# Optimization experiments

Hardware: AMD Instinct MI355X
Metric: run time of the kernel (lower is better)

The kernel has to match this reference:

```python
import jax, jax.numpy as jnp
import numpy as np

T, IN, INTER, OUT = 4096, 1024, 1024, 1024

def setup_inputs() -> dict:
    key = jax.random.key(0)
    ks = jax.random.split(key, 11)
    s_in = 1.0 / np.sqrt(IN)
    s_int = 1.0 / np.sqrt(INTER)
    return {
        "x": jax.random.normal(ks[0], (T, IN), dtype=jnp.float32),
        "d_gamma": jax.random.uniform(ks[1], (T, T), dtype=jnp.float32),
        "Wq": jax.random.uniform(ks[2], (IN, INTER), jnp.float32, -s_in, s_in),
        "bq": jax.random.uniform(ks[3], (INTER,), jnp.float32, -s_in, s_in),
        "Wk": jax.random.uniform(ks[4], (IN, INTER), jnp.float32, -s_in, s_in),
        "bk": jax.random.uniform(ks[5], (INTER,), jnp.float32, -s_in, s_in),
        "Wv": jax.random.uniform(ks[6], (IN, INTER), jnp.float32, -s_in, s_in),
        "bv": jax.random.uniform(ks[7], (INTER,), jnp.float32, -s_in, s_in),
        "Wr": jax.random.uniform(ks[8], (INTER, OUT), jnp.float32, -s_int, s_int),
        "br": jax.random.uniform(ks[9], (OUT,), jnp.float32, -s_int, s_int),
        "prelu_a": jnp.asarray(0.25, dtype=jnp.float32),
    }

def reference(x, d_gamma, Wq, bq, Wk, bk, Wv, bv, Wr, br, prelu_a):
    num_node = x.shape[0]
    xr = x.reshape(T, IN)
    q = xr @ Wq + bq                      # [T, INTER]
    k = xr @ Wk + bk                      # [T, INTER]
    v = xr @ Wv + bv                      # [T, INTER]
    scores = q @ k.T                      # [T, T] retention scores
    retained = (d_gamma * scores) @ v     # decay-masked aggregation, [T, INTER]
    out = retained @ Wr + br              # [T, OUT]
    out = jnp.where(out >= 0, out, prelu_a * out)  # PReLU
    return out.reshape(num_node, -1)
```

## Files before the change

kernel.cpp:

```cpp
#include <hip/hip_runtime.h>

#define TT 4096
#define DIN 1024

typedef _Float16 f16;
typedef __attribute__((ext_vector_type(8))) _Float16 f16x8;
typedef __attribute__((ext_vector_type(4))) _Float16 f16x4;
typedef __attribute__((ext_vector_type(4))) float f32x4;

__device__ f16 g_xh[TT * DIN];
__device__ f16 g_wqkvT[3 * DIN * DIN];
__device__ f16 g_wrT[DIN * DIN];
__device__ f16 g_q[TT * DIN];
__device__ f16 g_k[TT * DIN];
__device__ f16 g_v[TT * DIN];
__device__ f16 g_vT[DIN * TT];
__device__ f16 g_sg[(size_t)TT * TT];
__device__ f16 g_part[4][TT * DIN];
__device__ f16 g_ret[TT * DIN];

__global__ __launch_bounds__(256) void prep_cast_x(const float* __restrict__ x) {
    int i = (blockIdx.x * 256 + threadIdx.x) * 8;
    f32x4 a = *(const f32x4*)&x[i];
    f32x4 b = *(const f32x4*)&x[i + 4];
    f16x8 o;
#pragma unroll
    for (int j = 0; j < 4; ++j) { o[j] = (f16)a[j]; o[j + 4] = (f16)b[j]; }
    *(f16x8*)&g_xh[i] = o;
}

__global__ __launch_bounds__(256) void prep_transpose(const float* __restrict__ Wq,
                                                      const float* __restrict__ Wk,
                                                      const float* __restrict__ Wv,
                                                      const float* __restrict__ Wr) {
    __shared__ float tt[64][68];
    const int which = blockIdx.z;
    const float* src = (which == 0) ? Wq : (which == 1) ? Wk : (which == 2) ? Wv : Wr;
    f16* dst = (which < 3) ? (g_wqkvT + (size_t)which * DIN * DIN) : g_wrT;
    const int t = threadIdx.x;
    const int r = t >> 2;
    const int c0 = (t & 3) * 4;
#pragma unroll
    for (int ch = 0; ch < 4; ++ch)
        *(f32x4*)&tt[r][c0 + ch * 16] =
            *(const f32x4*)&src[(size_t)(blockIdx.y * 64 + r) * DIN + blockIdx.x * 64 + c0 + ch * 16];
    __syncthreads();
#pragma unroll
    for (int p = 0; p < 2; ++p) {
        const int j  = (t >> 3) + p * 32;
        const int k0 = (t & 7) * 8;
        f16x8 o;
#pragma unroll
        for (int jj = 0; jj < 8; ++jj) o[jj] = (f16)tt[k0 + jj][j];
        *(f16x8*)&dst[(size_t)(blockIdx.x * 64 + j) * DIN + blockIdx.y * 64 + k0] = o;
    }
}

__global__ __launch_bounds__(256) void transpose_v() {
    __shared__ f16 t[64][72];
    const int bc = blockIdx.x;
    const int br = blockIdx.y;
    const int tdx = threadIdx.x;
    const int r0 = tdx >> 3;
    const int c8 = (tdx & 7) * 8;
#pragma unroll
    for (int p = 0; p < 2; ++p) {
        int r = r0 + p * 32;
        *(f16x8*)&t[r][c8] = *(const f16x8*)&g_v[(size_t)(br * 64 + r) * DIN + bc * 64 + c8];
    }
    __syncthreads();
#pragma unroll
    for (int p = 0; p < 2; ++p) {
        int c = r0 + p * 32;
        f16x8 v;
#pragma unroll
        for (int j = 0; j < 8; ++j) v[j] = t[c8 + j][c];
        *(f16x8*)&g_vT[(size_t)(bc * 64 + c) * TT + br * 64 + c8] = v;
    }
}

__device__ __forceinline__ void gload_lds16(const void* g, void* l) {
    __builtin_amdgcn_global_load_lds(
        (const __attribute__((address_space(1))) unsigned int*)g,
        (__attribute__((address_space(3))) unsigned int*)l,
        16, 0, 0);
}

template <int EPI>
__global__ __launch_bounds__(512, 2) void gemm8(const float* __restrict__ gamma,
                                                const float* __restrict__ bq,
                                                const float* __restrict__ bk,
                                                const float* __restrict__ bv) {
    constexpr int NT  = (EPI == 3) ? 4 : 16;
    constexpr int ld2A = (EPI == 2) ? 8192 : 2048;
    constexpr int ld2B = (EPI == 2) ? 8192 : 2048;

    const f16* Ap = (EPI == 0) ? g_xh : (EPI == 1) ? g_q : (EPI == 2) ? g_sg : g_ret;
    const f16* Bp = (EPI == 0) ? g_wqkvT : (EPI == 1) ? g_k : (EPI == 2) ? g_vT : g_wrT;
    const int kb_base = (EPI == 2) ? blockIdx.z * 2048
                      : (EPI == 3) ? blockIdx.z * 512 : 0;

    __shared__ __align__(16) char smem[131072];

    const int t = threadIdx.x;
    const int w = t >> 6, l = t & 63;
    const int wr = w >> 2, wc = w & 3;
    const int fr = l & 15;
    const int fkb = (l >> 4) * 16;

    const int nx = gridDim.x;
    const int lin = blockIdx.y * nx + blockIdx.x;
    const int cpx = (nx * gridDim.y) >> 3;
    const int sw = (lin & 7) * cpx + (lin >> 3);
    const int bx = sw % nx, by = sw / nx;
    const int arow0 = by * 256;
    const int bcol0 = bx * 256;

    auto stage = [&](const f16* M, int ld2, int row0, int kb0, int dstoff) {
#pragma unroll
        for (int r = 0; r < 2; ++r) {
            int off = r * 8192 + w * 1024;
            int row = (off + l * 16) >> 7;
            int cb  = (l & 7) * 16;
            int scb = cb ^ ((row & 7) << 4);
            const char* src = (const char*)M + (size_t)(row0 + row) * ld2 + kb0 + scb;
            gload_lds16(src, smem + dstoff + off);
        }
    };

    auto ldsA = [&](int c, int m, int ks) -> f16x8 {
        int lr = m * 16 + fr;
        int kb = ks * 64 + fkb;
        return *(const f16x8*)(smem + c * 65536 + wr * 16384 + lr * 128 + (kb ^ ((lr & 7) << 4)));
    };
    auto ldsB = [&](int c, int n, int ks) -> f16x8 {
        int lc = (wc & 1) * 64 + n * 16 + fr;
        int kb = ks * 64 + fkb;
        return *(const f16x8*)(smem + c * 65536 + 32768 + (wc >> 1) * 16384 + lc * 128 + (kb ^ ((lc & 7) << 4)));
    };

#define KB(kt) (kb_base + (kt) * 128)

    stage(Ap, ld2A, arow0,       KB(0), 0);
    stage(Ap, ld2A, arow0 + 128, KB(0), 16384);
    stage(Bp, ld2B, bcol0,       KB(0), 32768);
    stage(Bp, ld2B, bcol0 + 128, KB(0), 49152);
    stage(Bp, ld2B, bcol0,       KB(1), 65536 + 32768);
    stage(Bp, ld2B, bcol0 + 128, KB(1), 65536 + 49152);

    f32x4 acc[8][4] = {};
    f16x8 bf[4][2];

#define GPHASE(MB, STAGE_STMT)                                              \
    {                                                                       \
        f16x8 af[2][2];                                                     \
        _Pragma("unroll") for (int i = 0; i < 2; ++i)                       \
            _Pragma("unroll") for (int ks = 0; ks < 2; ++ks)                \
                af[i][ks] = ldsA(c, (MB) + i, ks);                          \
        STAGE_STMT;                                                         \
        __builtin_amdgcn_s_barrier();                                       \
        __builtin_amdgcn_s_setprio(1);                                      \
        _Pragma("unroll") for (int i = 0; i < 2; ++i)                       \
            _Pragma("unroll") for (int n = 0; n < 4; ++n)                   \
                _Pragma("unroll") for (int ks = 0; ks < 2; ++ks)            \
                    acc[(MB) + i][n] = __builtin_amdgcn_mfma_f32_16x16x32_f16( \
                        af[i][ks], bf[n][ks], acc[(MB) + i][n], 0, 0, 0);   \
        __builtin_amdgcn_s_setprio(0);                                      \
        __builtin_amdgcn_s_barrier();                                       \
    }

    for (int kt = 0; kt < NT; ++kt) {
        const int c = kt & 1;
        if (kt == NT - 1) asm volatile("s_waitcnt vmcnt(0)" ::: "memory");
        else              asm volatile("s_waitcnt vmcnt(4)" ::: "memory");
        __builtin_amdgcn_s_barrier();
#pragma unroll
        for (int n = 0; n < 4; ++n)
#pragma unroll
            for (int ks = 0; ks < 2; ++ks) bf[n][ks] = ldsB(c, n, ks);
        GPHASE(0, if (kt + 1 < NT) stage(Ap, ld2A, arow0,       KB(kt + 1), (c ^ 1) * 65536))
        GPHASE(2, if (kt + 1 < NT) stage(Ap, ld2A, arow0 + 128, KB(kt + 1), (c ^ 1) * 65536 + 16384))
        GPHASE(4, if (kt + 2 < NT) stage(Bp, ld2B, bcol0,       KB(kt + 2), c * 65536 + 32768))
        GPHASE(6, if (kt + 2 < NT) stage(Bp, ld2B, bcol0 + 128, KB(kt + 2), c * 65536 + 49152))
    }
#undef GPHASE
#undef KB

    __syncthreads();
    char* slice = smem + w * 16384;
    const int rb = (l >> 4) * 4;
    const int crow0 = arow0 + wr * 128;
    const int ccol0 = bcol0 + wc * 64;

    const int sel = (EPI == 0) ? (bx >> 2) : 0;
    const float* bias0 = (EPI == 0) ? ((sel == 0) ? bq : (sel == 1) ? bk : bv) : nullptr;
    const int cb0 = (EPI == 0) ? (ccol0 - sel * 1024) : ccol0;

#pragma unroll
    for (int m = 0; m < 8; ++m)
#pragma unroll
        for (int n = 0; n < 4; ++n) {
            float bsum = 0.f;
            if constexpr (EPI == 0) bsum = bias0[cb0 + n * 16 + fr];
#pragma unroll
            for (int j = 0; j < 4; ++j) {
                const int lr = m * 16 + rb + j;
                const int lcb = (n * 16 + fr) * 2;
                *(f16*)(slice + lr * 128 + (lcb ^ ((lr & 7) << 4))) = (f16)(acc[m][n][j] + bsum);
            }
        }
    asm volatile("s_waitcnt lgkmcnt(0)" ::: "memory");
    __builtin_amdgcn_sched_barrier(0);

    if constexpr (EPI == 1) {
#pragma unroll 1
        for (int g = 0; g < 2; ++g) {
            f32x4 ga[8][2];
#pragma unroll
            for (int i = 0; i < 8; ++i) {
                const int r = (g * 8 + i) * 8 + (l >> 3);
                const float* gp = &gamma[(size_t)(crow0 + r) * TT + ccol0 + (l & 7) * 8];
                ga[i][0] = *(const f32x4*)gp;
                ga[i][1] = *(const f32x4*)(gp + 4);
            }
#pragma unroll
            for (int i = 0; i < 8; ++i) {
                const int r  = (g * 8 + i) * 8 + (l >> 3);
                const int cb = (l & 7) * 16;
                f16x8 vv = *(const f16x8*)(slice + r * 128 + (cb ^ ((r & 7) << 4)));
                f16x8 o;
#pragma unroll
                for (int j = 0; j < 4; ++j) {
                    o[j]     = (f16)((float)vv[j] * ga[i][0][j]);
                    o[j + 4] = (f16)((float)vv[j + 4] * ga[i][1][j]);
                }
                *(f16x8*)&g_sg[(size_t)(crow0 + r) * TT + ccol0 + (l & 7) * 8] = o;
            }
        }
    } else {
        f16* dst;
        int ld;
        if constexpr (EPI == 0) { dst = (sel == 0) ? g_q : (sel == 1) ? g_k : g_v; ld = 1024; }
        else                    { dst = g_part[blockIdx.z]; ld = 1024; }
#pragma unroll
        for (int i = 0; i < 16; ++i) {
            const int r  = i * 8 + (l >> 3);
            const int cb = (l & 7) * 16;
            f16x8 vv = *(const f16x8*)(slice + r * 128 + (cb ^ ((r & 7) << 4)));
            *(f16x8*)&dst[(size_t)(crow0 + r) * ld + cb0 + (l & 7) * 8] = vv;
        }
    }
}

__global__ __launch_bounds__(256) void reduce_parts() {
    size_t i = (size_t)(blockIdx.x * 256 + threadIdx.x) * 8;
    f16x8 a = *(const f16x8*)&g_part[0][i];
    f16x8 b = *(const f16x8*)&g_part[1][i];
    f16x8 cc = *(const f16x8*)&g_part[2][i];
    f16x8 d = *(const f16x8*)&g_part[3][i];
    f16x8 o;
#pragma unroll
    for (int j = 0; j < 8; ++j)
        o[j] = (f16)((float)a[j] + (float)b[j] + (float)cc[j] + (float)d[j]);
    *(f16x8*)&g_ret[i] = o;
}

__global__ __launch_bounds__(256) void reduce_out(const float* __restrict__ br,
                                                  const float* __restrict__ prelu_a,
                                                  float* __restrict__ out) {
    size_t i = (size_t)(blockIdx.x * 256 + threadIdx.x) * 8;
    f16x8 a = *(const f16x8*)&g_part[0][i];
    f16x8 b = *(const f16x8*)&g_part[1][i];
    f16x8 cc = *(const f16x8*)&g_part[2][i];
    f16x8 d = *(const f16x8*)&g_part[3][i];
    const float pa = *prelu_a;
    const int col = (int)(i & 1023);
    const f32x4 b0 = *(const f32x4*)&br[col];
    const f32x4 b1 = *(const f32x4*)&br[col + 4];
    f32x4 o0, o1;
#pragma unroll
    for (int j = 0; j < 4; ++j) {
        float s = (float)a[j] + (float)b[j] + (float)cc[j] + (float)d[j] + b0[j];
        o0[j] = (s >= 0.f) ? s : pa * s;
    }
#pragma unroll
    for (int j = 0; j < 4; ++j) {
        float s = (float)a[j + 4] + (float)b[j + 4] + (float)cc[j + 4] + (float)d[j + 4] + b1[j];
        o1[j] = (s >= 0.f) ? s : pa * s;
    }
    *(f32x4*)&out[i] = o0;
    *(f32x4*)&out[i + 4] = o1;
}

extern "C" void kernel_launch(void* const* d_in, const int* in_sizes, int n_in,
                              void* d_out, int out_size, void* d_ws, size_t ws_size,
                              hipStream_t stream) {
    const float* x     = (const float*)d_in[0];
    const float* gamma = (const float*)d_in[1];
    const float* Wq    = (const float*)d_in[2];
    const float* bq    = (const float*)d_in[3];
    const float* Wk    = (const float*)d_in[4];
    const float* bk    = (const float*)d_in[5];
    const float* Wv    = (const float*)d_in[6];
    const float* bv    = (const float*)d_in[7];
    const float* Wr    = (const float*)d_in[8];
    const float* br    = (const float*)d_in[9];
    const float* pa    = (const float*)d_in[10];
    float* out = (float*)d_out;

    prep_cast_x<<<TT * DIN / 8 / 256, 256, 0, stream>>>(x);
    prep_transpose<<<dim3(16, 16, 4), 256, 0, stream>>>(Wq, Wk, Wv, Wr);

    gemm8<0><<<dim3(12, 16), 512, 0, stream>>>(gamma, bq, bk, bv);
    transpose_v<<<dim3(16, 64), 256, 0, stream>>>();
    gemm8<1><<<dim3(16, 16), 512, 0, stream>>>(gamma, bq, bk, bv);
    gemm8<2><<<dim3(4, 16, 4), 512, 0, stream>>>(gamma, bq, bk, bv);
    reduce_parts<<<TT * DIN / 8 / 256, 256, 0, stream>>>();
    gemm8<3><<<dim3(4, 16, 4), 512, 0, stream>>>(gamma, bq, bk, bv);
    reduce_out<<<TT * DIN / 8 / 256, 256, 0, stream>>>(br, pa, out);
}
```

Baseline: 177.1 us.

## Move decay-mask multiply from scores epilogue into retained GEMM A-loads

The scores GEMM now writes raw q·kᵀ to the fp16 buffer, and the gamma multiply moves into the A-tile load path of the following (S∘γ)·V GEMM. That GEMM fetches the fp16 scores and fp32 gamma into registers, multiplies them and writes the product to LDS, with explicit vmcnt waits interleaved into the pipelined phases. This frees the scores epilogue from reading gamma, but every split-K block of the second GEMM now reads gamma and uses register-staged loads instead of direct global-to-LDS copies, which adds register pressure and could hurt overlap.

```diff
diff --git a/kernel.cpp b/kernel.cpp
--- a/kernel.cpp
+++ b/kernel.cpp
@@ -128,6 +128,36 @@
         }
     };
 
+    f16x8 sA[2][2];
+    f32x4 gA[2][2][2];
+    auto issueA = [&](int half, int kb0) {
+#pragma unroll
+        for (int r = 0; r < 2; ++r) {
+            int off = r * 8192 + w * 1024;
+            int row = (off + l * 16) >> 7;
+            int cb  = (l & 7) * 16;
+            int scb = cb ^ ((row & 7) << 4);
+            size_t ecol = (size_t)(kb_base + kb0 + scb) >> 1;
+            size_t base = (size_t)(arow0 + half * 128 + row) * 4096 + ecol;
+            sA[half][r]    = *(const f16x8*)&g_sg[base];
+            gA[half][r][0] = *(const f32x4*)&gamma[base];
+            gA[half][r][1] = *(const f32x4*)&gamma[base + 4];
+        }
+    };
+    auto writeA = [&](int half, int dstoff) {
+#pragma unroll
+        for (int r = 0; r < 2; ++r) {
+            int off = r * 8192 + w * 1024 + l * 16;
+            f16x8 o;
+#pragma unroll
+            for (int j = 0; j < 4; ++j) {
+                o[j]     = (f16)((float)sA[half][r][j]     * gA[half][r][0][j]);
+                o[j + 4] = (f16)((float)sA[half][r][j + 4] * gA[half][r][1][j]);
+            }
+            *(f16x8*)(smem + dstoff + off) = o;
+        }
+    };
+
     auto ldsA = [&](int c, int m, int ks) -> f16x8 {
         int lr = m * 16 + fr;
         int kb = ks * 64 + fkb;
@@ -140,16 +170,30 @@
     };
 
 #define KB(kt) (kb_base + (kt) * 128)
-
-    stage(Ap, ld2A, arow0,       KB(0), 0);
-    stage(Ap, ld2A, arow0 + 128, KB(0), 16384);
-    stage(Bp, ld2B, bcol0,       KB(0), 32768);
-    stage(Bp, ld2B, bcol0 + 128, KB(0), 49152);
-    stage(Bp, ld2B, bcol0,       KB(1), 65536 + 32768);
-    stage(Bp, ld2B, bcol0 + 128, KB(1), 65536 + 49152);
+#define KBL(kt) ((kt) * 128)
 
     f32x4 acc[8][4] = {};
     f16x8 bf[4][2];
+
+    if constexpr (EPI == 2) {
+        issueA(0, KBL(0));
+        issueA(1, KBL(0));
+        stage(Bp, ld2B, bcol0,       KB(0), 32768);
+        stage(Bp, ld2B, bcol0 + 128, KB(0), 49152);
+        stage(Bp, ld2B, bcol0,       KB(1), 65536 + 32768);
+        stage(Bp, ld2B, bcol0 + 128, KB(1), 65536 + 49152);
+        asm volatile("s_waitcnt vmcnt(8)" ::: "memory");
+        writeA(0, 0);
+        writeA(1, 16384);
+        asm volatile("s_waitcnt lgkmcnt(0)" ::: "memory");
+    } else {
+        stage(Ap, ld2A, arow0,       KB(0), 0);
+        stage(Ap, ld2A, arow0 + 128, KB(0), 16384);
+        stage(Bp, ld2B, bcol0,       KB(0), 32768);
+        stage(Bp, ld2B, bcol0 + 128, KB(0), 49152);
+        stage(Bp, ld2B, bcol0,       KB(1), 65536 + 32768);
+        stage(Bp, ld2B, bcol0 + 128, KB(1), 65536 + 49152);
+    }
 
 #define GPHASE(MB, STAGE_STMT)                                              \
     {                                                                       \
@@ -178,13 +222,36 @@
         for (int n = 0; n < 4; ++n)
 #pragma unroll
             for (int ks = 0; ks < 2; ++ks) bf[n][ks] = ldsB(c, n, ks);
-        GPHASE(0, if (kt + 1 < NT) stage(Ap, ld2A, arow0,       KB(kt + 1), (c ^ 1) * 65536))
-        GPHASE(2, if (kt + 1 < NT) stage(Ap, ld2A, arow0 + 128, KB(kt + 1), (c ^ 1) * 65536 + 16384))
-        GPHASE(4, if (kt + 2 < NT) stage(Bp, ld2B, bcol0,       KB(kt + 2), c * 65536 + 32768))
-        GPHASE(6, if (kt + 2 < NT) stage(Bp, ld2B, bcol0 + 128, KB(kt + 2), c * 65536 + 49152))
+        if constexpr (EPI == 2) {
+            GPHASE(0, if (kt + 1 < NT) issueA(0, KBL(kt + 1)))
+            GPHASE(2, if (kt + 1 < NT) issueA(1, KBL(kt + 1)))
+            GPHASE(4, {
+                if (kt + 1 < NT) {
+                    asm volatile("s_waitcnt vmcnt(6)" ::: "memory");
+                    writeA(0, (c ^ 1) * 65536);
+                    asm volatile("s_waitcnt lgkmcnt(0)" ::: "memory");
+                }
+                if (kt + 2 < NT) stage(Bp, ld2B, bcol0, KB(kt + 2), c * 65536 + 32768);
+            })
+            GPHASE(6, {
+                if (kt + 2 < NT) asm volatile("s_waitcnt vmcnt(2)" ::: "memory");
+                else             asm volatile("s_waitcnt vmcnt(0)" ::: "memory");
+                if (kt + 1 < NT) {
+                    writeA(1, (c ^ 1) * 65536 + 16384);
+                    asm volatile("s_waitcnt lgkmcnt(0)" ::: "memory");
+                }
+                if (kt + 2 < NT) stage(Bp, ld2B, bcol0 + 128, KB(kt + 2), c * 65536 + 49152);
+            })
+        } else {
+            GPHASE(0, if (kt + 1 < NT) stage(Ap, ld2A, arow0,       KB(kt + 1), (c ^ 1) * 65536))
+            GPHASE(2, if (kt + 1 < NT) stage(Ap, ld2A, arow0 + 128, KB(kt + 1), (c ^ 1) * 65536 + 16384))
+            GPHASE(4, if (kt + 2 < NT) stage(Bp, ld2B, bcol0,       KB(kt + 2), c * 65536 + 32768))
+            GPHASE(6, if (kt + 2 < NT) stage(Bp, ld2B, bcol0 + 128, KB(kt + 2), c * 65536 + 49152))
+        }
     }
 #undef GPHASE
 #undef KB
+#undef KBL
 
     __syncthreads();
     char* slice = smem + w * 16384;
@@ -212,43 +279,17 @@
     asm volatile("s_waitcnt lgkmcnt(0)" ::: "memory");
     __builtin_amdgcn_sched_barrier(0);
 
-    if constexpr (EPI == 1) {
-#pragma unroll 1
-        for (int g = 0; g < 2; ++g) {
-            f32x4 ga[8][2];
-#pragma unroll
-            for (int i = 0; i < 8; ++i) {
-                const int r = (g * 8 + i) * 8 + (l >> 3);
-                const float* gp = &gamma[(size_t)(crow0 + r) * TT + ccol0 + (l & 7) * 8];
-                ga[i][0] = *(const f32x4*)gp;
-                ga[i][1] = *(const f32x4*)(gp + 4);
-            }
-#pragma unroll
-            for (int i = 0; i < 8; ++i) {
-                const int r  = (g * 8 + i) * 8 + (l >> 3);
-                const int cb = (l & 7) * 16;
-                f16x8 vv = *(const f16x8*)(slice + r * 128 + (cb ^ ((r & 7) << 4)));
-                f16x8 o;
-#pragma unroll
-                for (int j = 0; j < 4; ++j) {
-                    o[j]     = (f16)((float)vv[j] * ga[i][0][j]);
-                    o[j + 4] = (f16)((float)vv[j + 4] * ga[i][1][j]);
-                }
-                *(f16x8*)&g_sg[(size_t)(crow0 + r) * TT + ccol0 + (l & 7) * 8] = o;
-            }
-        }
-    } else {
-        f16* dst;
-        int ld;
-        if constexpr (EPI == 0) { dst = (sel == 0) ? g_q : (sel == 1) ? g_k : g_v; ld = 1024; }
-        else                    { dst = g_part[blockIdx.z]; ld = 1024; }
-#pragma unroll
-        for (int i = 0; i < 16; ++i) {
-            const int r  = i * 8 + (l >> 3);
-            const int cb = (l & 7) * 16;
-            f16x8 vv = *(const f16x8*)(slice + r * 128 + (cb ^ ((r & 7) << 4)));
-            *(f16x8*)&dst[(size_t)(crow0 + r) * ld + cb0 + (l & 7) * 8] = vv;
-        }
+    f16* dst;
+    int ld;
+    if constexpr (EPI == 0)      { dst = (sel == 0) ? g_q : (sel == 1) ? g_k : g_v; ld = 1024; }
+    else if constexpr (EPI == 1) { dst = g_sg;               ld = TT;   }
+    else                         { dst = g_part[blockIdx.z]; ld = 1024; }
+#pragma unroll
+    for (int i = 0; i < 16; ++i) {
+        const int r  = i * 8 + (l >> 3);
+        const int cb = (l & 7) * 16;
+        f16x8 vv = *(const f16x8*)(slice + r * 128 + (cb ^ ((r & 7) << 4)));
+        *(f16x8*)&dst[(size_t)(crow0 + r) * ld + cb0 + (l & 7) * 8] = vv;
     }
 }
 
```

Result: slower. 184.1 us (+4.0%).

## Fuse QK^T, gamma decay and PV into one retention kernel

Applied to the files above, without the earlier changes.

Replaces the separate score GEMM (with gamma epilogue writing a TxT fp16 matrix) and the split-K PV GEMM with a single kernel. Each block computes 64x256 score tiles in registers, scales by gamma, stages them in LDS and immediately multiplies by V^T tiles, accumulating partial outputs per j-quarter. This removes the large score matrix round trip through global memory. In exchange it uses small tiles, 160KB LDS limiting occupancy, and full vmcnt waits that reduce load/compute overlap.

```diff
diff --git a/kernel.cpp b/kernel.cpp
--- a/kernel.cpp
+++ b/kernel.cpp
@@ -15,7 +15,6 @@
 __device__ f16 g_k[TT * DIN];
 __device__ f16 g_v[TT * DIN];
 __device__ f16 g_vT[DIN * TT];
-__device__ f16 g_sg[(size_t)TT * TT];
 __device__ f16 g_part[4][TT * DIN];
 __device__ f16 g_ret[TT * DIN];
 
@@ -87,18 +86,13 @@
 }
 
 template <int EPI>
-__global__ __launch_bounds__(512, 2) void gemm8(const float* __restrict__ gamma,
-                                                const float* __restrict__ bq,
+__global__ __launch_bounds__(512, 2) void gemm8(const float* __restrict__ bq,
                                                 const float* __restrict__ bk,
                                                 const float* __restrict__ bv) {
-    constexpr int NT  = (EPI == 3) ? 4 : 16;
-    constexpr int ld2A = (EPI == 2) ? 8192 : 2048;
-    constexpr int ld2B = (EPI == 2) ? 8192 : 2048;
-
-    const f16* Ap = (EPI == 0) ? g_xh : (EPI == 1) ? g_q : (EPI == 2) ? g_sg : g_ret;
-    const f16* Bp = (EPI == 0) ? g_wqkvT : (EPI == 1) ? g_k : (EPI == 2) ? g_vT : g_wrT;
-    const int kb_base = (EPI == 2) ? blockIdx.z * 2048
-                      : (EPI == 3) ? blockIdx.z * 512 : 0;
+    constexpr int NT = (EPI == 3) ? 4 : 16;
+    const f16* Ap = (EPI == 0) ? g_xh : g_ret;
+    const f16* Bp = (EPI == 0) ? g_wqkvT : g_wrT;
+    const int kb_base = (EPI == 3) ? blockIdx.z * 512 : 0;
 
     __shared__ __align__(16) char smem[131072];
 
@@ -116,18 +110,16 @@
     const int arow0 = by * 256;
     const int bcol0 = bx * 256;
 
-    auto stage = [&](const f16* M, int ld2, int row0, int kb0, int dstoff) {
+    auto stage = [&](const f16* M, int row0, int kb0, int dstoff) {
 #pragma unroll
         for (int r = 0; r < 2; ++r) {
             int off = r * 8192 + w * 1024;
             int row = (off + l * 16) >> 7;
-            int cb  = (l & 7) * 16;
-            int scb = cb ^ ((row & 7) << 4);
-            const char* src = (const char*)M + (size_t)(row0 + row) * ld2 + kb0 + scb;
+            int scb = ((l & 7) * 16) ^ ((row & 7) << 4);
+            const char* src = (const char*)M + (size_t)(row0 + row) * 2048 + kb0 + scb;
             gload_lds16(src, smem + dstoff + off);
         }
     };
-
     auto ldsA = [&](int c, int m, int ks) -> f16x8 {
         int lr = m * 16 + fr;
         int kb = ks * 64 + fkb;
@@ -140,13 +132,12 @@
     };
 
 #define KB(kt) (kb_base + (kt) * 128)
-
-    stage(Ap, ld2A, arow0,       KB(0), 0);
-    stage(Ap, ld2A, arow0 + 128, KB(0), 16384);
-    stage(Bp, ld2B, bcol0,       KB(0), 32768);
-    stage(Bp, ld2B, bcol0 + 128, KB(0), 49152);
-    stage(Bp, ld2B, bcol0,       KB(1), 65536 + 32768);
-    stage(Bp, ld2B, bcol0 + 128, KB(1), 65536 + 49152);
+    stage(Ap, arow0,       KB(0), 0);
+    stage(Ap, arow0 + 128, KB(0), 16384);
+    stage(Bp, bcol0,       KB(0), 32768);
+    stage(Bp, bcol0 + 128, KB(0), 49152);
+    stage(Bp, bcol0,       KB(1), 65536 + 32768);
+    stage(Bp, bcol0 + 128, KB(1), 65536 + 49152);
 
     f32x4 acc[8][4] = {};
     f16x8 bf[4][2];
@@ -178,10 +169,10 @@
         for (int n = 0; n < 4; ++n)
 #pragma unroll
             for (int ks = 0; ks < 2; ++ks) bf[n][ks] = ldsB(c, n, ks);
-        GPHASE(0, if (kt + 1 < NT) stage(Ap, ld2A, arow0,       KB(kt + 1), (c ^ 1) * 65536))
-        GPHASE(2, if (kt + 1 < NT) stage(Ap, ld2A, arow0 + 128, KB(kt + 1), (c ^ 1) * 65536 + 16384))
-        GPHASE(4, if (kt + 2 < NT) stage(Bp, ld2B, bcol0,       KB(kt + 2), c * 65536 + 32768))
-        GPHASE(6, if (kt + 2 < NT) stage(Bp, ld2B, bcol0 + 128, KB(kt + 2), c * 65536 + 49152))
+        GPHASE(0, if (kt + 1 < NT) stage(Ap, arow0,       KB(kt + 1), (c ^ 1) * 65536))
+        GPHASE(2, if (kt + 1 < NT) stage(Ap, arow0 + 128, KB(kt + 1), (c ^ 1) * 65536 + 16384))
+        GPHASE(4, if (kt + 2 < NT) stage(Bp, bcol0,       KB(kt + 2), c * 65536 + 32768))
+        GPHASE(6, if (kt + 2 < NT) stage(Bp, bcol0 + 128, KB(kt + 2), c * 65536 + 49152))
     }
 #undef GPHASE
 #undef KB
@@ -212,43 +203,175 @@
     asm volatile("s_waitcnt lgkmcnt(0)" ::: "memory");
     __builtin_amdgcn_sched_barrier(0);
 
-    if constexpr (EPI == 1) {
+    f16* dst;
+    if constexpr (EPI == 0) dst = (sel == 0) ? g_q : (sel == 1) ? g_k : g_v;
+    else                    dst = g_part[blockIdx.z];
+#pragma unroll
+    for (int i = 0; i < 16; ++i) {
+        const int r  = i * 8 + (l >> 3);
+        const int cb = (l & 7) * 16;
+        f16x8 vv = *(const f16x8*)(slice + r * 128 + (cb ^ ((r & 7) << 4)));
+        *(f16x8*)&dst[(size_t)(crow0 + r) * 1024 + cb0 + (l & 7) * 8] = vv;
+    }
+}
+
+__global__ __launch_bounds__(512, 2) void fused_ret(const float* __restrict__ gamma) {
+    const int t = threadIdx.x;
+    const int w = t >> 6, l = t & 63;
+    const int fr = l & 15;
+    const int fkb = (l >> 4) * 16;
+    const int rb = (l >> 4) * 4;
+    const int qt64 = blockIdx.x * 64;
+    const int jbase = blockIdx.y * 1024;
+    f16* gp = g_part[blockIdx.y];
+
+    __shared__ __align__(16) char smem[163840];
+    constexpr int QB0 = 32768, KB0 = 40960, QB1 = 98304, KB1 = 106496;
+    constexpr int VB0 = 32768, VB1 = 98304;
+
+    auto stageQ = [&](int kstep, int qb) {
+        int row = w * 8 + (l >> 3);
+        int scb = ((l & 7) * 16) ^ ((row & 7) << 4);
+        const char* src = (const char*)g_q + (size_t)(qt64 + row) * 2048 + kstep * 128 + scb;
+        gload_lds16(src, smem + qb + w * 1024);
+    };
+    auto stageK = [&](int jt, int kstep, int kb) {
+#pragma unroll
+        for (int i = 0; i < 4; ++i) {
+            int row = i * 64 + w * 8 + (l >> 3);
+            int scb = ((l & 7) * 16) ^ ((row & 7) << 4);
+            const char* src = (const char*)g_k + (size_t)(jbase + jt * 256 + row) * 2048 + kstep * 128 + scb;
+            gload_lds16(src, smem + kb + i * 8192 + w * 1024);
+        }
+    };
+    auto stageV = [&](int jt, int s, int vb) {
+#pragma unroll
+        for (int i = 0; i < 8; ++i) {
+            int row = i * 128 + w * 16 + (l >> 2);
+            int ssb = ((l & 3) * 16) ^ ((row & 3) << 4);
+            const char* src = (const char*)g_vT + (size_t)row * 8192
+                              + (size_t)(jbase + jt * 256 + s * 32) * 2 + ssb;
+            gload_lds16(src, smem + vb + i * 8192 + w * 1024);
+        }
+    };
+
+    f32x4 acc[4][8] = {};
+
 #pragma unroll 1
-        for (int g = 0; g < 2; ++g) {
-            f32x4 ga[8][2];
-#pragma unroll
-            for (int i = 0; i < 8; ++i) {
-                const int r = (g * 8 + i) * 8 + (l >> 3);
-                const float* gp = &gamma[(size_t)(crow0 + r) * TT + ccol0 + (l & 7) * 8];
-                ga[i][0] = *(const f32x4*)gp;
-                ga[i][1] = *(const f32x4*)(gp + 4);
-            }
-#pragma unroll
-            for (int i = 0; i < 8; ++i) {
-                const int r  = (g * 8 + i) * 8 + (l >> 3);
-                const int cb = (l & 7) * 16;
-                f16x8 vv = *(const f16x8*)(slice + r * 128 + (cb ^ ((r & 7) << 4)));
-                f16x8 o;
-#pragma unroll
-                for (int j = 0; j < 4; ++j) {
-                    o[j]     = (f16)((float)vv[j] * ga[i][0][j]);
-                    o[j + 4] = (f16)((float)vv[j + 4] * ga[i][1][j]);
+    for (int jt = 0; jt < 4; ++jt) {
+        f32x4 accS[2][4] = {};
+        stageQ(0, QB0); stageK(jt, 0, KB0);
+#pragma unroll 1
+        for (int kt = 0; kt < 16; ++kt) {
+            asm volatile("s_waitcnt vmcnt(0)" ::: "memory");
+            __builtin_amdgcn_s_barrier();
+            const int qb = (kt & 1) ? QB1 : QB0;
+            const int kb = (kt & 1) ? KB1 : KB0;
+            f16x8 af[2][2], bf[4][2];
+#pragma unroll
+            for (int m = 0; m < 2; ++m)
+#pragma unroll
+                for (int ks = 0; ks < 2; ++ks) {
+                    int row = (w & 1) * 32 + m * 16 + fr;
+                    af[m][ks] = *(const f16x8*)(smem + qb + row * 128 + ((ks * 64 + fkb) ^ ((row & 7) << 4)));
                 }
-                *(f16x8*)&g_sg[(size_t)(crow0 + r) * TT + ccol0 + (l & 7) * 8] = o;
-            }
-        }
-    } else {
-        f16* dst;
-        int ld;
-        if constexpr (EPI == 0) { dst = (sel == 0) ? g_q : (sel == 1) ? g_k : g_v; ld = 1024; }
-        else                    { dst = g_part[blockIdx.z]; ld = 1024; }
-#pragma unroll
-        for (int i = 0; i < 16; ++i) {
-            const int r  = i * 8 + (l >> 3);
-            const int cb = (l & 7) * 16;
-            f16x8 vv = *(const f16x8*)(slice + r * 128 + (cb ^ ((r & 7) << 4)));
-            *(f16x8*)&dst[(size_t)(crow0 + r) * ld + cb0 + (l & 7) * 8] = vv;
-        }
+#pragma unroll
+            for (int n = 0; n < 4; ++n)
+#pragma unroll
+                for (int ks = 0; ks < 2; ++ks) {
+                    int row = (w >> 1) * 64 + n * 16 + fr;
+                    bf[n][ks] = *(const f16x8*)(smem + kb + row * 128 + ((ks * 64 + fkb) ^ ((row & 7) << 4)));
+                }
+            if (kt + 1 < 16) {
+                stageQ(kt + 1, (kt & 1) ? QB0 : QB1);
+                stageK(jt, kt + 1, (kt & 1) ? KB0 : KB1);
+            }
+            __builtin_amdgcn_s_barrier();
+            __builtin_amdgcn_s_setprio(1);
+#pragma unroll
+            for (int m = 0; m < 2; ++m)
+#pragma unroll
+                for (int n = 0; n < 4; ++n)
+#pragma unroll
+                    for (int ks = 0; ks < 2; ++ks)
+                        accS[m][n] = __builtin_amdgcn_mfma_f32_16x16x32_f16(af[m][ks], bf[n][ks], accS[m][n], 0, 0, 0);
+            __builtin_amdgcn_s_setprio(0);
+        }
+        float gv[2][4][4];
+#pragma unroll
+        for (int m = 0; m < 2; ++m)
+#pragma unroll
+            for (int n = 0; n < 4; ++n) {
+                const int scol = (w >> 1) * 64 + n * 16 + fr;
+#pragma unroll
+                for (int jj = 0; jj < 4; ++jj) {
+                    const int srow = (w & 1) * 32 + m * 16 + rb + jj;
+                    gv[m][n][jj] = gamma[(size_t)(qt64 + srow) * TT + jbase + jt * 256 + scol];
+                }
+            }
+#pragma unroll
+        for (int m = 0; m < 2; ++m)
+#pragma unroll
+            for (int n = 0; n < 4; ++n) {
+                const int scol = (w >> 1) * 64 + n * 16 + fr;
+#pragma unroll
+                for (int jj = 0; jj < 4; ++jj) {
+                    const int srow = (w & 1) * 32 + m * 16 + rb + jj;
+                    *(f16*)(smem + srow * 512 + ((scol * 2) ^ ((srow & 7) << 4))) =
+                        (f16)(accS[m][n][jj] * gv[m][n][jj]);
+                }
+            }
+        asm volatile("s_waitcnt lgkmcnt(0)" ::: "memory");
+        __builtin_amdgcn_sched_barrier(0);
+        __builtin_amdgcn_s_barrier();
+        stageV(jt, 0, VB0);
+#pragma unroll 1
+        for (int s = 0; s < 8; ++s) {
+            asm volatile("s_waitcnt vmcnt(0)" ::: "memory");
+            __builtin_amdgcn_s_barrier();
+            const int vb = (s & 1) ? VB1 : VB0;
+            f16x8 saf[4], vbf[8];
+#pragma unroll
+            for (int m = 0; m < 4; ++m) {
+                int row = m * 16 + fr;
+                saf[m] = *(const f16x8*)(smem + row * 512 + ((s * 64 + fkb) ^ ((row & 7) << 4)));
+            }
+#pragma unroll
+            for (int n = 0; n < 8; ++n) {
+                int row = w * 128 + n * 16 + fr;
+                vbf[n] = *(const f16x8*)(smem + vb + row * 64 + (fkb ^ ((row & 3) << 4)));
+            }
+            if (s + 1 < 8) stageV(jt, s + 1, (s & 1) ? VB0 : VB1);
+            __builtin_amdgcn_s_barrier();
+            __builtin_amdgcn_s_setprio(1);
+#pragma unroll
+            for (int m = 0; m < 4; ++m)
+#pragma unroll
+                for (int n = 0; n < 8; ++n)
+                    acc[m][n] = __builtin_amdgcn_mfma_f32_16x16x32_f16(saf[m], vbf[n], acc[m][n], 0, 0, 0);
+            __builtin_amdgcn_s_setprio(0);
+        }
+        __builtin_amdgcn_s_barrier();
+    }
+    char* slice = smem + w * 16384;
+#pragma unroll
+    for (int m = 0; m < 4; ++m)
+#pragma unroll
+        for (int n = 0; n < 8; ++n)
+#pragma unroll
+            for (int jj = 0; jj < 4; ++jj) {
+                const int lr = m * 16 + rb + jj;
+                const int lcb = (n * 16 + fr) * 2;
+                *(f16*)(slice + lr * 256 + (lcb ^ ((lr & 7) << 4))) = (f16)acc[m][n][jj];
+            }
+    asm volatile("s_waitcnt lgkmcnt(0)" ::: "memory");
+    __builtin_amdgcn_sched_barrier(0);
+#pragma unroll
+    for (int i = 0; i < 16; ++i) {
+        const int r  = i * 4 + (l >> 4);
+        const int cb = (l & 15) * 16;
+        f16x8 vv = *(const f16x8*)(slice + r * 256 + (cb ^ ((r & 7) << 4)));
+        *(f16x8*)&gp[(size_t)(qt64 + r) * 1024 + w * 128 + (l & 15) * 8] = vv;
     }
 }
 
@@ -311,11 +434,10 @@
     prep_cast_x<<<TT * DIN / 8 / 256, 256, 0, stream>>>(x);
     prep_transpose<<<dim3(16, 16, 4), 256, 0, stream>>>(Wq, Wk, Wv, Wr);
 
-    gemm8<0><<<dim3(12, 16), 512, 0, stream>>>(gamma, bq, bk, bv);
+    gemm8<0><<<dim3(12, 16), 512, 0, stream>>>(bq, bk, bv);
     transpose_v<<<dim3(16, 64), 256, 0, stream>>>();
-    gemm8<1><<<dim3(16, 16), 512, 0, stream>>>(gamma, bq, bk, bv);
-    gemm8<2><<<dim3(4, 16, 4), 512, 0, stream>>>(gamma, bq, bk, bv);
+    fused_ret<<<dim3(64, 4), 512, 0, stream>>>(gamma);
     reduce_parts<<<TT * DIN / 8 / 256, 256, 0, stream>>>();
-    gemm8<3><<<dim3(4, 16, 4), 512, 0, stream>>>(gamma, bq, bk, bv);
+    gemm8<3><<<dim3(4, 16, 4), 512, 0, stream>>>(bq, bk, bv);
     reduce_out<<<TT * DIN / 8 / 256, 256, 0, stream>>>(br, pa, out);
 }
```

Measured after the change: 276.2 us. 56.0% more time.
